# Kernel tuning notes

Measured on AMD Instinct MI355X. Metric: run time of the kernel, lower is better.

The kernel has to match this reference:

```python
import jax, jax.numpy as jnp
from jax import lax
import numpy as np
import math

KSIZE, STRIDE, RATE, FUSE_K, SCALE, FUSE = 3, 1, 2, 3, 10.0, True
DN = ('NCHW', 'OIHW', 'NCHW')


def extract_image_patches(img, kernel, stride=1):
    # Faithful to the torch helper, including the F.pad quirk where pad_row
    # (computed from height) is applied to the width axis and vice versa.
    bsz, c, h, w = img.shape
    h2 = math.ceil(h / stride)
    w2 = math.ceil(w / stride)
    pad_row = (h2 - 1) * stride + kernel - h
    pad_col = (w2 - 1) * stride + kernel - w
    x = jnp.pad(img, ((0, 0), (0, 0),
                      (pad_col // 2, pad_col - pad_col // 2),
                      (pad_row // 2, pad_row - pad_row // 2)))
    cols = []
    for i in range(kernel):
        for j in range(kernel):
            cols.append(x[:, :, i:i + (h2 - 1) * stride + 1:stride,
                          j:j + (w2 - 1) * stride + 1:stride])
    patches = jnp.stack(cols, axis=-1).reshape(bsz, c, h2, w2, kernel, kernel)
    patches = jnp.transpose(patches, (0, 4, 5, 1, 2, 3))  # [b,kh,kw,c,h2,w2]
    return patches.reshape(bsz, -1, h2, w2)


def setup_inputs() -> dict:
    key = jax.random.key(0)
    k1, k2, k3 = jax.random.split(key, 3)
    f = jax.random.normal(k1, (4, 128, 96, 96), dtype=jnp.float32)
    b = jax.random.normal(k2, (4, 128, 96, 96), dtype=jnp.float32)
    mask = jax.random.uniform(k3, (4, 1, 96, 96), dtype=jnp.float32)
    return {'f': f, 'b': b, 'mask': mask}


def reference(f, b, mask):
    bs, cs, hs, ws = f.shape
    kernel = RATE * 2
    # raw background patches used as conv_transpose filters (C-order reshape as in torch .view)
    raw_w = extract_image_patches(b, kernel, RATE * STRIDE)
    raw_w = raw_w.reshape(bs, -1, kernel, kernel, cs).transpose(0, 1, 4, 2, 3)  # [bs,L,cs,4,4]
    # nearest downsample by rate (matches F.interpolate nearest with scale 1/rate)
    fd = f[:, :, ::RATE, ::RATE]
    bd = b[:, :, ::RATE, ::RATE]
    md = mask[:, :, ::RATE, ::RATE]
    ih, iw = bd.shape[2], bd.shape[3]
    L = ih * iw
    w = extract_image_patches(bd, KSIZE, STRIDE)
    w = w.reshape(bs, -1, KSIZE, KSIZE, cs).transpose(0, 1, 4, 2, 3)  # [bs,L,cs,3,3]
    m = extract_image_patches(md, KSIZE, STRIDE)
    m = m.reshape(bs, -1, 1, KSIZE, KSIZE).transpose(0, 2, 3, 4, 1)  # [bs,1,3,3,L]
    mms = (jnp.mean(1.0 - m, axis=(1, 2, 3)) < 0.85).astype(f.dtype)  # [bs,L]
    fuse_w = jnp.eye(FUSE_K, dtype=f.dtype).reshape(1, 1, FUSE_K, FUSE_K)

    def per_sample(xi, wi, raw_wi, mm):
        # xi [cs,ih,iw], wi [L,cs,3,3], raw_wi [L,cs,4,4], mm [L]
        norm = jnp.sqrt(jnp.sum(wi * wi, axis=(1, 2, 3)) + 1e-8)
        wi_n = wi / jnp.maximum(norm, 1e-4)[:, None, None, None]
        yi = lax.conv_general_dilated(xi[None], wi_n, (1, 1), ((1, 1), (1, 1)),
                                      dimension_numbers=DN)  # [1,L,ih,iw]
        if FUSE:
            yi = yi.reshape(1, 1, ih * iw, ih * iw)
            yi = lax.conv_general_dilated(yi, fuse_w, (1, 1), ((1, 1), (1, 1)), dimension_numbers=DN)
            yi = yi.reshape(1, ih, iw, ih, iw).transpose(0, 2, 1, 4, 3)
            yi = yi.reshape(1, 1, ih * iw, ih * iw)
            yi = lax.conv_general_dilated(yi, fuse_w, (1, 1), ((1, 1), (1, 1)), dimension_numbers=DN)
            yi = yi.reshape(1, iw, ih, iw, ih).transpose(0, 2, 1, 4, 3)
        yi = yi.reshape(1, ih, iw, iw * ih)
        yi = yi * mm
        yi = jax.nn.softmax(yi * SCALE, axis=3)
        yi = yi * mm
        off = jnp.argmax(yi, axis=3).astype(jnp.int32)
        off = jnp.stack([off // hs, off % hs], axis=-1).transpose(0, 3, 1, 2)  # [1,2,ih,iw]
        yi = yi.transpose(0, 3, 1, 2)  # [1,L,ih,iw]
        # conv_transpose2d(yi, raw_wi, stride=RATE, padding=1) == dilated corr with flipped, transposed kernel
        w_t = jnp.flip(raw_wi, (-2, -1)).transpose(1, 0, 2, 3)  # [cs,L,4,4]
        pad = kernel - 1 - 1
        out = lax.conv_general_dilated(yi, w_t, (1, 1), ((pad, pad), (pad, pad)),
                                       lhs_dilation=(RATE, RATE), dimension_numbers=DN) / 4.0
        return out[0], off[0]

    y, offsets = jax.vmap(per_sample)(fd, w, raw_w, mms)  # y [bs,cs,hs,ws], offsets [bs,2,ih,iw]
    grid = jnp.stack([jnp.broadcast_to(jnp.arange(ih)[:, None], (ih, iw)),
                      jnp.broadcast_to(jnp.arange(iw)[None, :], (ih, iw))], 0).astype(jnp.int32)
    offsets = offsets - grid[None]
    # flow_to_image (external numpy visualization) omitted; raw offsets returned instead.
    return y, offsets
```

## Files before the change

### kernel.cpp

```cpp
#include <hip/hip_runtime.h>
#include <hip/hip_bf16.h>
#include <math.h>

#define IH 48
#define IW 48
#define LTOT 2304
#define CS 128
#define HS 96
#define KRED 1152
#define CRED 2048

typedef unsigned short u16;
typedef __attribute__((ext_vector_type(8))) short short8;
typedef __attribute__((ext_vector_type(8))) unsigned short ushort8;
typedef __attribute__((ext_vector_type(4))) float floatx4;

#define NS    ((size_t)LTOT*LTOT)
#define PLANE ((size_t)LTOT*KRED)

#define OFF_APL  ((size_t)0)
#define OFF_BPL  ((size_t)10616832)
#define OFF_S    ((size_t)21233664)
#define OFF_C    ((size_t)42467328)
#define OFF_SM   ((size_t)61341696)
#define REGION   ((size_t)61360128)

__device__ __forceinline__ u16 f2bf(float v) {
    __hip_bfloat16 h = __float2bfloat16(v);
    return *reinterpret_cast<u16*>(&h);
}
__device__ __forceinline__ float bf2f(u16 b) {
    __hip_bfloat16 h = *reinterpret_cast<__hip_bfloat16*>(&b);
    return __bfloat162float(h);
}
__device__ __forceinline__ void split2(float v, u16& a, u16& b) {
    a = f2bf(v);
    b = f2bf(v - bf2f(a));
}

__global__ __launch_bounds__(256) void k_wnorm(const float* __restrict__ b,
                                               float* __restrict__ ninvg,
                                               int b0, size_t zsF) {
    int bi = b0 + blockIdx.z;
    float* ninv = ninvg + (size_t)blockIdx.z * zsF;
    int l = blockIdx.x, t = threadIdx.x;
    __shared__ float red[256];
    float ss = 0.f;
    for (int G = t; G < KRED; G += 256) {
        int F = l * KRED + G;
        int p2 = F / LTOT, s = F - p2 * LTOT;
        int i = p2 / 384, j = (p2 / 128) % 3, c = p2 & 127;
        int u = s / IW + i - 1, v = s % IW + j - 1;
        if (u >= 0 && u < IH && v >= 0 && v < IW) {
            float w = b[(((size_t)bi * CS + c) * HS + 2 * u) * HS + 2 * v];
            ss += w * w;
        }
    }
    red[t] = ss; __syncthreads();
    for (int o = 128; o > 0; o >>= 1) { if (t < o) red[t] += red[t + o]; __syncthreads(); }
    if (t == 0) ninv[l] = 1.0f / fmaxf(sqrtf(red[0] + 1e-8f), 1e-4f);
}

__global__ __launch_bounds__(256) void k_gather_w(const float* __restrict__ b,
                                                  u16* __restrict__ Ag,
                                                  const float* __restrict__ ninvg,
                                                  int b0, size_t zsU, size_t zsF) {
    int bi = b0 + blockIdx.z;
    u16* A = Ag + (size_t)blockIdx.z * zsU;
    const float* ninv = ninvg + (size_t)blockIdx.z * zsF;
    int idx = blockIdx.x * 256 + threadIdx.x;
    int p2 = idx / LTOT, s = idx - p2 * LTOT;
    int i = p2 / 384, j = (p2 / 128) % 3, c = p2 & 127;
    int u = s / IW + i - 1, v = s % IW + j - 1;
    float val = 0.f;
    if (u >= 0 && u < IH && v >= 0 && v < IW)
        val = b[(((size_t)bi * CS + c) * HS + 2 * u) * HS + 2 * v];
    val *= ninv[idx / KRED];
    u16 h1, h2; split2(val, h1, h2);
    A[idx] = h1; A[PLANE + idx] = h2;
}

__global__ __launch_bounds__(256) void k_gather_x_tiled(const float* __restrict__ f,
                                                        u16* __restrict__ Bg,
                                                        int b0, size_t zsU) {
    __shared__ float ldsf[128 * 55];
    int bi = b0 + blockIdx.z;
    u16* B = Bg + (size_t)blockIdx.z * zsU;
    int bx = blockIdx.x;
    int y = bx / 3, x0 = (bx % 3) * 16;
    int t = threadIdx.x;
    for (int i = 0; i < 27; ++i) {
        int g = i * 256 + t;
        if (g < 6912) {
            int vl = g % 18;
            int row = (g / 18) % 3;
            int c = g / 54;
            int u = y + row - 1;
            int v = x0 - 1 + vl;
            float val = 0.f;
            if (u >= 0 && u < IH && v >= 0 && v < IW)
                val = f[(((size_t)bi * CS + c) * HS + 2 * u) * HS + 2 * v];
            ldsf[c * 55 + row * 18 + vl] = val;
        }
    }
    __syncthreads();
    for (int i = 0; i < 72; ++i) {
        int o = i * 256 + t;
        int xp = o / 1152, G = o - xp * 1152;
        int k1 = G / 384, k2 = (G >> 7) % 3, c = G & 127;
        float val = ldsf[c * 55 + k1 * 18 + xp + k2];
        u16 h1, h2; split2(val, h1, h2);
        size_t idx = (size_t)(y * IW + x0 + xp) * KRED + G;
        B[idx] = h1; B[PLANE + idx] = h2;
    }
}

__global__ __launch_bounds__(256) void k_mm(const float* __restrict__ mask,
                                            float* __restrict__ mmvg, int b0, size_t zsF) {
    int bi = b0 + blockIdx.z;
    float* out = mmvg + (size_t)blockIdx.z * zsF;
    int q = blockIdx.x * 256 + threadIdx.x;
    if (q >= LTOT) return;
    float ssum = 0.f;
    for (int t = 0; t < 9; t++) {
        int F = q * 9 + t;
        int pm = F / LTOT, s = F % LTOT;
        int i = pm / 3, j = pm % 3;
        int u = s / IW + i - 1, v = s % IW + j - 1;
        float val = 0.f;
        if (u >= 0 && u < IH && v >= 0 && v < IW)
            val = mask[((size_t)bi * HS + 2 * u) * HS + 2 * v];
        ssum += 1.0f - val;
    }
    out[q] = (ssum / 9.0f < 0.85f) ? 1.0f : 0.0f;
}

template <int NP, int BK>
__global__ __launch_bounds__(256) void k_gemm_mfma(const u16* __restrict__ Ag,
                                                   const u16* __restrict__ Bg,
                                                   float* __restrict__ Cg,
                                                   size_t zsA, size_t zsB, size_t zsC,
                                                   size_t planeStride,
                                                   int M, int N, int K) {
    constexpr int SLOTS = BK / 8;
    constexpr int SMASK = SLOTS - 1;
    constexpr int TSZ = 128 * BK;
    constexpr int NLD = NP * BK / 16;
    __shared__ u16 lds[2 * NP * TSZ];
    u16* As = lds;
    u16* Bs = lds + NP * TSZ;
    const int tid = threadIdx.x;
    const int lane = tid & 63;
    const int wave = tid >> 6;
    const int wr = (wave >> 1) * 64, wc = (wave & 1) * 64;
    const int lrow = lane & 15, lq = lane >> 4;

    unsigned gx = gridDim.x, gy = gridDim.y;
    unsigned nwg = gx * gy * gridDim.z;
    unsigned wg = (blockIdx.z * gy + blockIdx.y) * gx + blockIdx.x;
    {
        unsigned q = nwg >> 3, r = nwg & 7, xcd = wg & 7, lid = wg >> 3;
        wg = (xcd < r ? xcd * (q + 1) : r * (q + 1) + (xcd - r) * q) + lid;
    }
    unsigned z = wg / (gx * gy);
    unsigned rem2 = wg - z * gx * gy;
    const int bm = (int)(rem2 / gx) * 128, bn = (int)(rem2 % gx) * 128;

    const u16* A = Ag + (size_t)z * zsA;
    const u16* B = Bg + (size_t)z * zsB;
    float* C = Cg + (size_t)z * zsC;

    floatx4 acc[4][4];
#pragma unroll
    for (int i = 0; i < 4; i++)
#pragma unroll
        for (int j = 0; j < 4; j++) acc[i][j] = (floatx4){0.f, 0.f, 0.f, 0.f};

    for (int kt = 0; kt < K; kt += BK) {
        ushort8 stA[NLD], stB[NLD];
#pragma unroll
        for (int e = 0; e < NLD; ++e) {
            int g = e * 256 + tid;
            int p = g / (128 * SLOTS);
            int gg = g % (128 * SLOTS);
            int row = gg / SLOTS, slot = gg & SMASK;
            stA[e] = *(const ushort8*)(A + (size_t)p * planeStride + (size_t)(bm + row) * K + kt + slot * 8);
            stB[e] = *(const ushort8*)(B + (size_t)p * planeStride + (size_t)(bn + row) * K + kt + slot * 8);
        }
        __syncthreads();
#pragma unroll
        for (int e = 0; e < NLD; ++e) {
            int g = e * 256 + tid;
            int p = g / (128 * SLOTS);
            int gg = g % (128 * SLOTS);
            int row = gg / SLOTS, slot = gg & SMASK;
            int dst = p * TSZ + row * BK + ((slot ^ (row & SMASK)) << 3);
            *(ushort8*)&As[dst] = stA[e];
            *(ushort8*)&Bs[dst] = stB[e];
        }
        __syncthreads();

#pragma unroll
        for (int ks = 0; ks < BK / 32; ++ks) {
            short8 af[NP][4];
#pragma unroll
            for (int p = 0; p < NP; ++p)
#pragma unroll
                for (int mi = 0; mi < 4; ++mi) {
                    int row = wr + mi * 16 + lrow;
                    af[p][mi] = *(const short8*)&As[p * TSZ + row * BK + ((((ks << 2) | lq) ^ (row & SMASK)) << 3)];
                }
#pragma unroll
            for (int ni = 0; ni < 4; ++ni) {
                short8 bfr[NP];
                int rowb = wc + ni * 16 + lrow;
                int bslot = ((((ks << 2) | lq) ^ (rowb & SMASK)) << 3);
#pragma unroll
                for (int p = 0; p < NP; ++p)
                    bfr[p] = *(const short8*)&Bs[p * TSZ + rowb * BK + bslot];
#pragma unroll
                for (int mi = 0; mi < 4; ++mi) {
                    if constexpr (NP == 1) {
                        acc[mi][ni] = __builtin_amdgcn_mfma_f32_16x16x32_bf16(af[0][mi], bfr[0], acc[mi][ni], 0, 0, 0);
                    } else {
                        acc[mi][ni] = __builtin_amdgcn_mfma_f32_16x16x32_bf16(af[1][mi], bfr[0], acc[mi][ni], 0, 0, 0);
                        acc[mi][ni] = __builtin_amdgcn_mfma_f32_16x16x32_bf16(af[0][mi], bfr[1], acc[mi][ni], 0, 0, 0);
                        acc[mi][ni] = __builtin_amdgcn_mfma_f32_16x16x32_bf16(af[0][mi], bfr[0], acc[mi][ni], 0, 0, 0);
                    }
                }
            }
        }
    }

    const int r0 = bm + wr + (lane >> 4) * 4;
    const int c0 = bn + wc + (lane & 15);
#pragma unroll
    for (int mi = 0; mi < 4; ++mi)
#pragma unroll
        for (int ni = 0; ni < 4; ++ni)
#pragma unroll
            for (int j = 0; j < 4; ++j)
                C[(size_t)(r0 + mi * 16 + j) * N + (c0 + ni * 16)] = acc[mi][ni][j];
}

__device__ __forceinline__ int permi(int a) { return (a % 48) * 48 + a / 48; }

__device__ __forceinline__ float f1_at(const float* __restrict__ S, int a, int b) {
    float s = S[(size_t)a * LTOT + b];
    if (a >= 1 && b >= 1) s += S[(size_t)(a - 1) * LTOT + (b - 1)];
    if (a < LTOT - 1 && b < LTOT - 1) s += S[(size_t)(a + 1) * LTOT + (b + 1)];
    return s;
}

__global__ __launch_bounds__(256) void k_fusesoftmax(const float* __restrict__ Sg,
                                                     const float* __restrict__ mmg,
                                                     const float* __restrict__ bsrc,
                                                     float* __restrict__ Cg,
                                                     float* __restrict__ offout,
                                                     int b0, size_t zsF) {
    int z = blockIdx.z;
    int bi = b0 + z;
    const float* S = Sg + (size_t)z * zsF;
    const float* mm = mmg + (size_t)z * zsF;
    float* C = Cg + (size_t)z * zsF;
    int bx = blockIdx.x;
    int l = (bx & 7) * 288 + (bx >> 3);
    int t = threadIdx.x;
    __shared__ float red[256];
    __shared__ int redi[256];
    __shared__ int scand[2304];
    __shared__ float swght[2304];
    __shared__ int scnt;
    if (t == 0) scnt = 0;

    const int At = permi(l);
    const int rm = (At >= 1) ? permi(At - 1) : -1;
    const int rp = (At < LTOT - 1) ? permi(At + 1) : -1;

    float v[9], m9[9];
#pragma unroll
    for (int i = 0; i < 9; ++i) {
        int p = t + 256 * i;
        float d = f1_at(S, l, p);
        int Bt = permi(p);
        if (rm >= 0 && Bt >= 1)        d += f1_at(S, rm, permi(Bt - 1));
        if (rp >= 0 && Bt < LTOT - 1)  d += f1_at(S, rp, permi(Bt + 1));
        m9[i] = mm[p];
        v[i] = d * m9[i] * 10.0f;
    }
    float mx = -1e30f;
#pragma unroll
    for (int i = 0; i < 9; ++i) mx = fmaxf(mx, v[i]);
    red[t] = mx; __syncthreads();
    for (int o = 128; o > 0; o >>= 1) { if (t < o) red[t] = fmaxf(red[t], red[t + o]); __syncthreads(); }
    mx = red[0]; __syncthreads();
    float sm = 0.f;
#pragma unroll
    for (int i = 0; i < 9; ++i) sm += expf(v[i] - mx);
    red[t] = sm; __syncthreads();
    for (int o = 128; o > 0; o >>= 1) { if (t < o) red[t] += red[t + o]; __syncthreads(); }
    float Z = red[0]; __syncthreads();
    float mul = -1e30f;
#pragma unroll
    for (int i = 0; i < 9; ++i) if (m9[i] > 0.f) mul = fmaxf(mul, v[i]);
    red[t] = mul; __syncthreads();
    for (int o = 128; o > 0; o >>= 1) { if (t < o) red[t] = fmaxf(red[t], red[t + o]); __syncthreads(); }
    float mu = red[0]; __syncthreads();
    float bv = -1.0f; int bidx2 = 0;
#pragma unroll
    for (int i = 0; i < 9; ++i) {
        int p = t + 256 * i;
        float e = expf(v[i] - mx);
        float a = (e / Z) * m9[i];
        if (a > bv) { bv = a; bidx2 = p; }
        if (m9[i] > 0.f && v[i] >= mu - 20.0f) {
            int pos = atomicAdd(&scnt, 1);
            scand[pos] = p;
            swght[pos] = e / Z;
        }
    }
    red[t] = bv; redi[t] = bidx2; __syncthreads();
    for (int o = 128; o > 0; o >>= 1) {
        if (t < o) {
            if (red[t + o] > red[t] || (red[t + o] == red[t] && redi[t + o] < redi[t])) {
                red[t] = red[t + o]; redi[t] = redi[t + o];
            }
        }
        __syncthreads();
    }
    if (t == 0) {
        int off = redi[0];
        int ly = l / IW, lx = l % IW;
        offout[((size_t)bi * 2 + 0) * LTOT + l] = (float)(off / 96 - ly);
        offout[((size_t)bi * 2 + 1) * LTOT + l] = (float)(off % 96 - lx);
    }
    int cnt = scnt;
    float accv[8];
#pragma unroll
    for (int j = 0; j < 8; ++j) accv[j] = 0.f;
    for (int ci = 0; ci < cnt; ++ci) {
        int p = scand[ci];
        float w = swght[ci];
#pragma unroll
        for (int j = 0; j < 8; ++j) {
            int n = t + 256 * j;
            int F = p * CRED + n;
            int pr = F / LTOT, s = F - pr * LTOT;
            int ii = pr >> 9, jj = (pr >> 7) & 3, c = pr & 127;
            int Y0 = 2 * (s / IW) + ii - 1, X0 = 2 * (s % IW) + jj - 1;
            float val = 0.f;
            if (Y0 >= 0 && Y0 < HS && X0 >= 0 && X0 < HS)
                val = bsrc[(((size_t)bi * CS + c) * HS + Y0) * HS + X0];
            accv[j] += w * val;
        }
    }
    float* Crow = C + (size_t)l * CRED;
#pragma unroll
    for (int j = 0; j < 8; ++j) Crow[t + 256 * j] = accv[j] * 0.25f;
}

__global__ __launch_bounds__(256) void k_output_tiled(const float* __restrict__ Cg,
                                                      float* __restrict__ yout,
                                                      int b0, size_t zsF) {
    __shared__ float lo[64 * 129];
    int bi = b0 + blockIdx.z;
    const float* C = Cg + (size_t)blockIdx.z * zsF;
    int bx = blockIdx.x;
    int Y0 = (bx / 6) * 4, X0 = (bx % 6) * 16;
    int t = threadIdx.x;
    int c = t & 127;
    for (int i = 0; i < 32; ++i) {
        int pos = i * 2 + (t >> 7);
        int Y = Y0 + (pos >> 4), X = X0 + (pos & 15);
        float s = 0.f;
        int pu = (Y + 1) & 1, pv = (X + 1) & 1;
#pragma unroll
        for (int a = 0; a < 2; a++) {
            int u = pu + 2 * a;
            int ly2 = Y + 1 - u;
            if (ly2 < 0) continue;
            int ly = ly2 >> 1;
            if (ly >= IH) continue;
#pragma unroll
            for (int bb = 0; bb < 2; bb++) {
                int v = pv + 2 * bb;
                int lx2 = X + 1 - v;
                if (lx2 < 0) continue;
                int lx = lx2 >> 1;
                if (lx >= IW) continue;
                s += C[(size_t)(ly * IW + lx) * CRED + u * 512 + v * 128 + c];
            }
        }
        lo[pos * 129 + c] = s;
    }
    __syncthreads();
    for (int i = 0; i < 32; ++i) {
        int cc = i * 4 + (t >> 6);
        int pos = t & 63;
        float val = lo[pos * 129 + cc];
        int yl = pos >> 4, xl = pos & 15;
        yout[(((size_t)bi * CS + cc) * HS + Y0 + yl) * HS + X0 + xl] = val;
    }
}

extern "C" void kernel_launch(void* const* d_in, const int* in_sizes, int n_in,
                              void* d_out, int out_size, void* d_ws, size_t ws_size,
                              hipStream_t stream) {
    const float* f = (const float*)d_in[0];
    const float* b = (const float*)d_in[1];
    const float* mask = (const float*)d_in[2];
    float* yout = (float*)d_out;
    float* offout = yout + (size_t)4 * CS * HS * HS;

    int ZB, nloop;
    if (ws_size >= 4 * REGION)      { ZB = 4; nloop = 1; }
    else if (ws_size >= 2 * REGION) { ZB = 2; nloop = 2; }
    else                            { ZB = 1; nloop = 4; }

    char* base = (char*)d_ws;
    u16*   Apl  = (u16*)(base + OFF_APL);
    u16*   Bpl  = (u16*)(base + OFF_BPL);
    float* S    = (float*)(base + OFF_S);
    float* Cc   = (float*)(base + OFF_C);
    float* ninv = (float*)(base + OFF_SM);
    float* mmv  = ninv + LTOT;

    const size_t zsU = REGION / 2;
    const size_t zsF = REGION / 4;

    dim3 blk(256, 1, 1);
    const unsigned ghalf = (unsigned)(PLANE / 256);

    for (int it = 0; it < nloop; ++it) {
        int b0 = it * ZB;
        k_wnorm<<<dim3(LTOT, 1, ZB), blk, 0, stream>>>(b, ninv, b0, zsF);
        k_gather_w<<<dim3(ghalf, 1, ZB), blk, 0, stream>>>(b, Apl, ninv, b0, zsU, zsF);
        k_gather_x_tiled<<<dim3(IH * 3, 1, ZB), blk, 0, stream>>>(f, Bpl, b0, zsU);
        k_mm<<<dim3((LTOT + 255) / 256, 1, ZB), blk, 0, stream>>>(mask, mmv, b0, zsF);
        k_gemm_mfma<2, 64><<<dim3(LTOT / 128, LTOT / 128, ZB), blk, 0, stream>>>(
            Apl, Bpl, S, zsU, zsU, zsF, PLANE, LTOT, LTOT, KRED);
        k_fusesoftmax<<<dim3(LTOT, 1, ZB), blk, 0, stream>>>(S, mmv, b, Cc, offout, b0, zsF);
        k_output_tiled<<<dim3((HS / 4) * (HS / 16), 1, ZB), blk, 0, stream>>>(Cc, yout, b0, zsF);
    }
}
```

Before: 515.8 us.

## Fuse weight norm with gather and compute softmax only over candidates

Merges the weight-norm kernel and the weight gather into one kernel that keeps the gathered values in registers, so the source is read once and one launch is dropped. The fused softmax kernel no longer does full-row max and sum reductions. It works out the masked maximum and its argmax in a single reduction, uses the fact that masked-out entries have value zero to get the row max and their exponent sum in closed form, and takes exponentials only for the thresholded candidates. It also replaces the permutation lookups for neighbour indices with direct arithmetic and does the patch index math incrementally in the accumulation loop. It relies on the mask being zero or positive and accepts small numerical differences in the softmax normalisation.

```diff
diff --git a/kernel.cpp b/kernel.cpp
--- a/kernel.cpp
+++ b/kernel.cpp
@@ -38,46 +38,42 @@
     b = f2bf(v - bf2f(a));
 }
 
-__global__ __launch_bounds__(256) void k_wnorm(const float* __restrict__ b,
-                                               float* __restrict__ ninvg,
-                                               int b0, size_t zsF) {
+__global__ __launch_bounds__(256) void k_wgather(const float* __restrict__ b,
+                                                 u16* __restrict__ Ag,
+                                                 int b0, size_t zsU) {
     int bi = b0 + blockIdx.z;
-    float* ninv = ninvg + (size_t)blockIdx.z * zsF;
+    u16* A = Ag + (size_t)blockIdx.z * zsU;
     int l = blockIdx.x, t = threadIdx.x;
     __shared__ float red[256];
+    float myv[5];
     float ss = 0.f;
-    for (int G = t; G < KRED; G += 256) {
-        int F = l * KRED + G;
-        int p2 = F / LTOT, s = F - p2 * LTOT;
-        int i = p2 / 384, j = (p2 / 128) % 3, c = p2 & 127;
-        int u = s / IW + i - 1, v = s % IW + j - 1;
-        if (u >= 0 && u < IH && v >= 0 && v < IW) {
-            float w = b[(((size_t)bi * CS + c) * HS + 2 * u) * HS + 2 * v];
-            ss += w * w;
-        }
+#pragma unroll
+    for (int k = 0; k < 5; ++k) {
+        int G = t + 256 * k;
+        float val = 0.f;
+        if (G < KRED) {
+            int F = l * KRED + G;
+            int p2 = F / LTOT, s = F - p2 * LTOT;
+            int i = p2 / 384, j = (p2 / 128) % 3, c = p2 & 127;
+            int u = s / IW + i - 1, v = s % IW + j - 1;
+            if (u >= 0 && u < IH && v >= 0 && v < IW)
+                val = b[(((size_t)bi * CS + c) * HS + 2 * u) * HS + 2 * v];
+        }
+        myv[k] = val;
+        ss += val * val;
     }
     red[t] = ss; __syncthreads();
     for (int o = 128; o > 0; o >>= 1) { if (t < o) red[t] += red[t + o]; __syncthreads(); }
-    if (t == 0) ninv[l] = 1.0f / fmaxf(sqrtf(red[0] + 1e-8f), 1e-4f);
-}
-
-__global__ __launch_bounds__(256) void k_gather_w(const float* __restrict__ b,
-                                                  u16* __restrict__ Ag,
-                                                  const float* __restrict__ ninvg,
-                                                  int b0, size_t zsU, size_t zsF) {
-    int bi = b0 + blockIdx.z;
-    u16* A = Ag + (size_t)blockIdx.z * zsU;
-    const float* ninv = ninvg + (size_t)blockIdx.z * zsF;
-    int idx = blockIdx.x * 256 + threadIdx.x;
-    int p2 = idx / LTOT, s = idx - p2 * LTOT;
-    int i = p2 / 384, j = (p2 / 128) % 3, c = p2 & 127;
-    int u = s / IW + i - 1, v = s % IW + j - 1;
-    float val = 0.f;
-    if (u >= 0 && u < IH && v >= 0 && v < IW)
-        val = b[(((size_t)bi * CS + c) * HS + 2 * u) * HS + 2 * v];
-    val *= ninv[idx / KRED];
-    u16 h1, h2; split2(val, h1, h2);
-    A[idx] = h1; A[PLANE + idx] = h2;
+    float ninv = 1.0f / fmaxf(sqrtf(red[0] + 1e-8f), 1e-4f);
+#pragma unroll
+    for (int k = 0; k < 5; ++k) {
+        int G = t + 256 * k;
+        if (G < KRED) {
+            u16 h1, h2; split2(myv[k] * ninv, h1, h2);
+            size_t F = (size_t)l * KRED + G;
+            A[F] = h1; A[PLANE + F] = h2;
+        }
+    }
 }
 
 __global__ __launch_bounds__(256) void k_gather_x_tiled(const float* __restrict__ f,
@@ -266,92 +262,105 @@
     int bx = blockIdx.x;
     int l = (bx & 7) * 288 + (bx >> 3);
     int t = threadIdx.x;
-    __shared__ float red[256];
+    __shared__ float redv[256];
     __shared__ int redi[256];
     __shared__ int scand[2304];
-    __shared__ float swght[2304];
+    __shared__ float scv[2304];
     __shared__ int scnt;
-    if (t == 0) scnt = 0;
+    __shared__ int sAny;
+    if (t == 0) { scnt = 0; sAny = 0; }
 
     const int At = permi(l);
     const int rm = (At >= 1) ? permi(At - 1) : -1;
     const int rp = (At < LTOT - 1) ? permi(At + 1) : -1;
 
-    float v[9], m9[9];
+    float v[9];
+    bool mk[9];
+    int nMaskLoc = 0;
 #pragma unroll
     for (int i = 0; i < 9; ++i) {
         int p = t + 256 * i;
         float d = f1_at(S, l, p);
-        int Bt = permi(p);
-        if (rm >= 0 && Bt >= 1)        d += f1_at(S, rm, permi(Bt - 1));
-        if (rp >= 0 && Bt < LTOT - 1)  d += f1_at(S, rp, permi(Bt + 1));
-        m9[i] = mm[p];
-        v[i] = d * m9[i] * 10.0f;
-    }
-    float mx = -1e30f;
-#pragma unroll
-    for (int i = 0; i < 9; ++i) mx = fmaxf(mx, v[i]);
-    red[t] = mx; __syncthreads();
-    for (int o = 128; o > 0; o >>= 1) { if (t < o) red[t] = fmaxf(red[t], red[t + o]); __syncthreads(); }
-    mx = red[0]; __syncthreads();
-    float sm = 0.f;
-#pragma unroll
-    for (int i = 0; i < 9; ++i) sm += expf(v[i] - mx);
-    red[t] = sm; __syncthreads();
-    for (int o = 128; o > 0; o >>= 1) { if (t < o) red[t] += red[t + o]; __syncthreads(); }
-    float Z = red[0]; __syncthreads();
-    float mul = -1e30f;
-#pragma unroll
-    for (int i = 0; i < 9; ++i) if (m9[i] > 0.f) mul = fmaxf(mul, v[i]);
-    red[t] = mul; __syncthreads();
-    for (int o = 128; o > 0; o >>= 1) { if (t < o) red[t] = fmaxf(red[t], red[t + o]); __syncthreads(); }
-    float mu = red[0]; __syncthreads();
-    float bv = -1.0f; int bidx2 = 0;
+        if (rm >= 0 && p >= 1)
+            d += f1_at(S, rm, (p >= 48) ? p - 48 : 2255 + p);
+        if (rp >= 0 && p != 2303)
+            d += f1_at(S, rp, (p < 2256) ? p + 48 : p - 2255);
+        float m = mm[p];
+        mk[i] = (m > 0.f);
+        if (!mk[i]) nMaskLoc++;
+        v[i] = d * m * 10.0f;
+    }
+    float lmu = -1e30f; int lidx = 0x7fffffff;
 #pragma unroll
     for (int i = 0; i < 9; ++i) {
         int p = t + 256 * i;
-        float e = expf(v[i] - mx);
-        float a = (e / Z) * m9[i];
-        if (a > bv) { bv = a; bidx2 = p; }
-        if (m9[i] > 0.f && v[i] >= mu - 20.0f) {
+        if (mk[i] && v[i] > lmu) { lmu = v[i]; lidx = p; }
+    }
+    if (nMaskLoc) sAny = 1;
+    redv[t] = lmu; redi[t] = lidx; __syncthreads();
+    for (int o = 128; o > 0; o >>= 1) {
+        if (t < o) {
+            if (redv[t + o] > redv[t] || (redv[t + o] == redv[t] && redi[t + o] < redi[t])) {
+                redv[t] = redv[t + o]; redi[t] = redi[t + o];
+            }
+        }
+        __syncthreads();
+    }
+    float mu = redv[0];
+    int muIdx = redi[0];
+    int anyM = sAny;
+    __syncthreads();
+    redi[t] = nMaskLoc; __syncthreads();
+    for (int o = 128; o > 0; o >>= 1) { if (t < o) redi[t] += redi[t + o]; __syncthreads(); }
+    int nMask = redi[0];
+    __syncthreads();
+
+    float mx = anyM ? fmaxf(mu, 0.f) : mu;
+
+#pragma unroll
+    for (int i = 0; i < 9; ++i) {
+        int p = t + 256 * i;
+        if (mk[i] && v[i] >= mu - 20.0f) {
             int pos = atomicAdd(&scnt, 1);
             scand[pos] = p;
-            swght[pos] = e / Z;
-        }
-    }
-    red[t] = bv; redi[t] = bidx2; __syncthreads();
-    for (int o = 128; o > 0; o >>= 1) {
-        if (t < o) {
-            if (red[t + o] > red[t] || (red[t + o] == red[t] && redi[t + o] < redi[t])) {
-                red[t] = red[t + o]; redi[t] = redi[t + o];
-            }
-        }
-        __syncthreads();
-    }
+            scv[pos] = v[i];
+        }
+    }
+    __syncthreads();
+    int cnt = scnt;
+
+    float Z = (float)nMask * __expf(0.f - mx);
+    for (int ci = 0; ci < cnt; ++ci) Z += __expf(scv[ci] - mx);
+
     if (t == 0) {
-        int off = redi[0];
+        int bestp = (cnt > 0) ? muIdx : 0;
         int ly = l / IW, lx = l % IW;
-        offout[((size_t)bi * 2 + 0) * LTOT + l] = (float)(off / 96 - ly);
-        offout[((size_t)bi * 2 + 1) * LTOT + l] = (float)(off % 96 - lx);
-    }
-    int cnt = scnt;
+        offout[((size_t)bi * 2 + 0) * LTOT + l] = (float)(bestp / 96 - ly);
+        offout[((size_t)bi * 2 + 1) * LTOT + l] = (float)(bestp % 96 - lx);
+    }
+
     float accv[8];
 #pragma unroll
     for (int j = 0; j < 8; ++j) accv[j] = 0.f;
     for (int ci = 0; ci < cnt; ++ci) {
         int p = scand[ci];
-        float w = swght[ci];
+        float w = __expf(scv[ci] - mx) / Z;
+        int F0 = p * 2048 + t;
+        int pr = F0 / 2304;
+        int s = F0 - pr * 2304;
+        int srow = s / 48;
+        int scol = s - srow * 48;
 #pragma unroll
         for (int j = 0; j < 8; ++j) {
-            int n = t + 256 * j;
-            int F = p * CRED + n;
-            int pr = F / LTOT, s = F - pr * LTOT;
             int ii = pr >> 9, jj = (pr >> 7) & 3, c = pr & 127;
-            int Y0 = 2 * (s / IW) + ii - 1, X0 = 2 * (s % IW) + jj - 1;
+            int Y0 = 2 * srow + ii - 1, X0 = 2 * scol + jj - 1;
             float val = 0.f;
             if (Y0 >= 0 && Y0 < HS && X0 >= 0 && X0 < HS)
                 val = bsrc[(((size_t)bi * CS + c) * HS + Y0) * HS + X0];
             accv[j] += w * val;
+            scol += 16; if (scol >= 48) { scol -= 48; srow += 1; }
+            srow += 5;
+            s += 256; if (s >= 2304) { s -= 2304; pr += 1; srow -= 48; }
         }
     }
     float* Crow = C + (size_t)l * CRED;
@@ -422,19 +431,16 @@
     u16*   Bpl  = (u16*)(base + OFF_BPL);
     float* S    = (float*)(base + OFF_S);
     float* Cc   = (float*)(base + OFF_C);
-    float* ninv = (float*)(base + OFF_SM);
-    float* mmv  = ninv + LTOT;
+    float* mmv  = (float*)(base + OFF_SM);
 
     const size_t zsU = REGION / 2;
     const size_t zsF = REGION / 4;
 
     dim3 blk(256, 1, 1);
-    const unsigned ghalf = (unsigned)(PLANE / 256);
 
     for (int it = 0; it < nloop; ++it) {
         int b0 = it * ZB;
-        k_wnorm<<<dim3(LTOT, 1, ZB), blk, 0, stream>>>(b, ninv, b0, zsF);
-        k_gather_w<<<dim3(ghalf, 1, ZB), blk, 0, stream>>>(b, Apl, ninv, b0, zsU, zsF);
+        k_wgather<<<dim3(LTOT, 1, ZB), blk, 0, stream>>>(b, Apl, b0, zsU);
         k_gather_x_tiled<<<dim3(IH * 3, 1, ZB), blk, 0, stream>>>(f, Bpl, b0, zsU);
         k_mm<<<dim3((LTOT + 255) / 256, 1, ZB), blk, 0, stream>>>(mask, mmv, b0, zsF);
         k_gemm_mfma<2, 64><<<dim3(LTOT / 128, LTOT / 128, ZB), blk, 0, stream>>>(
```

Result: faster. 474.7 us (-8.0%).
